# Kernel optimization log

Hardware: AMD Instinct MI355X
Metric: run time of the kernel (lower is better)

## Reference

```python
import jax, jax.numpy as jnp
import numpy as np

EPS = 1e-5
BATCH = 2
VOX_H = 8  # grid resolution at depth - stages = 3


def conv_bn_relu(x, neigh, W, gamma, beta):
    # octree sparse conv: gather 27 neighbors per node, then GEMM
    N = neigh.shape[0]
    g = x[neigh].reshape(N, -1)              # [N, 27*Cin]
    y = g @ W                                # [N, Cout]
    mean = jnp.mean(y, axis=0)
    var = jnp.var(y, axis=0)
    y = (y - mean) * jax.lax.rsqrt(var + EPS) * gamma + beta
    return jax.nn.relu(y)


def octree_max_pool(x):
    # max over 8 sibling children -> parent node
    return x.reshape(-1, 8, x.shape[-1]).max(axis=1)


def setup_inputs() -> dict:
    key = jax.random.key(0)
    ks = jax.random.split(key, 8)
    N6, N5, N4, N3 = 524288, 65536, 8192, 1024
    inp = {
        "data": jax.random.normal(ks[0], (N6, 4), jnp.float32),
        "W0": jax.random.normal(ks[1], (108, 16), jnp.float32) * 0.1,
        "g0": jnp.ones((16,), jnp.float32),
        "b0": jnp.zeros((16,), jnp.float32),
        "W1": jax.random.normal(ks[2], (432, 32), jnp.float32) * 0.05,
        "g1": jnp.ones((32,), jnp.float32),
        "b1": jnp.zeros((32,), jnp.float32),
        "W2": jax.random.normal(ks[3], (864, 64), jnp.float32) * 0.05,
        "g2": jnp.ones((64,), jnp.float32),
        "b2": jnp.zeros((64,), jnp.float32),
        "neigh0": jax.random.randint(ks[4], (N6, 27), 0, N6, jnp.int32),
        "neigh1": jax.random.randint(ks[5], (N5, 27), 0, N5, jnp.int32),
        "neigh2": jax.random.randint(ks[6], (N4, 27), 0, N4, jnp.int32),
        "vox_idx": jnp.arange(N3, dtype=jnp.int32),
        "depth": 6,
    }
    return inp


def reference(data, W0, g0, b0, W1, g1, b1, W2, g2, b2,
              neigh0, neigh1, neigh2, vox_idx, depth):
    x = conv_bn_relu(data, neigh0, W0, g0, b0)
    x = octree_max_pool(x)
    x = conv_bn_relu(x, neigh1, W1, g1, b1)
    x = octree_max_pool(x)
    x = conv_bn_relu(x, neigh2, W2, g2, b2)
    x = octree_max_pool(x)                   # [N3, 64]
    # octree2voxel: scatter node features into dense grid per batch sample
    C = x.shape[-1]
    vox = jnp.zeros((BATCH * VOX_H ** 3, C), x.dtype).at[vox_idx].set(x)
    vox = vox.reshape(BATCH, VOX_H, VOX_H, VOX_H, C)
    return vox.transpose(0, 4, 1, 2, 3)      # [B, C, H, H, H]
```

## Files before the change

kernel.cpp:

```cpp
#include <hip/hip_runtime.h>

#define BN_EPS 1e-5f
#define NBUF 64

typedef float        f32x4 __attribute__((ext_vector_type(4)));
typedef float        f32x2 __attribute__((ext_vector_type(2)));
typedef unsigned int u32x2 __attribute__((ext_vector_type(2)));
typedef unsigned int u32x4 __attribute__((ext_vector_type(4)));

__device__ inline unsigned pack_bf16(float a, float b) {
    unsigned ua = __float_as_uint(a);
    unsigned ub = __float_as_uint(b);
    ua = (ua + 0x7fffu + ((ua >> 16) & 1u)) >> 16;
    ub = (ub + 0x7fffu + ((ub >> 16) & 1u)) >> 16;
    return ua | (ub << 16);
}
__device__ inline float bf_lo(unsigned u) { return __uint_as_float(u << 16); }
__device__ inline float bf_hi(unsigned u) { return __uint_as_float(u & 0xffff0000u); }

__global__ void __launch_bounds__(256) cast_bf16_kernel(
    const f32x4* __restrict__ in, u32x2* __restrict__ out, int n4)
{
    const int t = blockIdx.x * 256 + threadIdx.x;
    if (t >= n4) return;
    const f32x4 v = in[t];
    u32x2 r;
    r.x = pack_bf16(v.x, v.y);
    r.y = pack_bf16(v.z, v.w);
    out[t] = r;
}

__global__ void __launch_bounds__(256) conv0_kernel(
    const unsigned long long* __restrict__ xb, const int* __restrict__ neigh,
    const float* __restrict__ W, float* __restrict__ y,
    float* __restrict__ stats)
{
    __shared__ float Wlds[27 * 4 * 16];
    for (int i = threadIdx.x; i < 27 * 4 * 16; i += 256) Wlds[i] = W[i];
    __syncthreads();

    const int node = blockIdx.x * 256 + threadIdx.x;
    const int* nrow = neigh + (size_t)node * 27;

    int idx[27];
#pragma unroll
    for (int j = 0; j < 27; ++j) idx[j] = __builtin_nontemporal_load(nrow + j);

    float acc[16];
#pragma unroll
    for (int c = 0; c < 16; ++c) acc[c] = 0.f;

#pragma unroll
    for (int g = 0; g < 27; g += 9) {
        unsigned long long xr[9];
#pragma unroll
        for (int u = 0; u < 9; ++u)
            xr[u] = __hip_atomic_load(xb + idx[g + u], __ATOMIC_RELAXED,
                                      __HIP_MEMORY_SCOPE_AGENT);
#pragma unroll
        for (int u = 0; u < 9; ++u) {
            const int j = g + u;
            const unsigned lo = (unsigned)xr[u];
            const unsigned hi = (unsigned)(xr[u] >> 32);
            float xv[4];
            xv[0] = bf_lo(lo); xv[1] = bf_hi(lo);
            xv[2] = bf_lo(hi); xv[3] = bf_hi(hi);
#pragma unroll
            for (int kk = 0; kk < 4; ++kk) {
                const f32x4* wv = (const f32x4*)&Wlds[(j * 4 + kk) * 16];
#pragma unroll
                for (int c4 = 0; c4 < 4; ++c4) {
                    const f32x4 w = wv[c4];
                    acc[c4 * 4 + 0] = fmaf(xv[kk], w.x, acc[c4 * 4 + 0]);
                    acc[c4 * 4 + 1] = fmaf(xv[kk], w.y, acc[c4 * 4 + 1]);
                    acc[c4 * 4 + 2] = fmaf(xv[kk], w.z, acc[c4 * 4 + 2]);
                    acc[c4 * 4 + 3] = fmaf(xv[kk], w.w, acc[c4 * 4 + 3]);
                }
            }
        }
    }

    f32x4* yr = (f32x4*)(y + (size_t)node * 16);
#pragma unroll
    for (int c4 = 0; c4 < 4; ++c4) {
        f32x4 v = { acc[c4 * 4 + 0], acc[c4 * 4 + 1], acc[c4 * 4 + 2], acc[c4 * 4 + 3] };
        __builtin_nontemporal_store(v, yr + c4);
    }

    float* buf = stats + (blockIdx.x & (NBUF - 1)) * (2 * 16);
#pragma unroll
    for (int c = 0; c < 16; ++c) {
        float v = acc[c];
        float q = v * v;
#pragma unroll
        for (int off = 32; off > 0; off >>= 1) {
            v += __shfl_xor(v, off, 64);
            q += __shfl_xor(q, off, 64);
        }
        if ((threadIdx.x & 63) == 0) {
            atomicAdd(&buf[c], v);
            atomicAdd(&buf[16 + c], q);
        }
    }
}

__global__ void __launch_bounds__(256) conv1_kernel(
    const u32x4* __restrict__ xb, const int* __restrict__ neigh,
    const float* __restrict__ W, float* __restrict__ y,
    float* __restrict__ stats)
{
    __shared__ float Wlds[27 * 16 * 8];
    const int cobase = blockIdx.y * 8;

    for (int i = threadIdx.x; i < 27 * 16 * 8; i += 256) {
        int k = i >> 3, c = i & 7;
        Wlds[i] = W[k * 32 + cobase + c];
    }
    __syncthreads();

    const int node = blockIdx.x * 256 + threadIdx.x;
    const int* nrow = neigh + (size_t)node * 27;

    int idx[27];
#pragma unroll
    for (int j = 0; j < 27; ++j) idx[j] = __builtin_nontemporal_load(nrow + j);

    float acc[8];
#pragma unroll
    for (int c = 0; c < 8; ++c) acc[c] = 0.f;

#pragma unroll 1
    for (int g = 0; g < 27; g += 3) {
        u32x4 xa[3], xc[3];
#pragma unroll
        for (int u = 0; u < 3; ++u) {
            const size_t r = (size_t)idx[g + u] * 2;
            xa[u] = xb[r];
            xc[u] = xb[r + 1];
        }
#pragma unroll
        for (int u = 0; u < 3; ++u) {
            const int j = g + u;
            float xv[16];
            xv[0]  = bf_lo(xa[u].x); xv[1]  = bf_hi(xa[u].x);
            xv[2]  = bf_lo(xa[u].y); xv[3]  = bf_hi(xa[u].y);
            xv[4]  = bf_lo(xa[u].z); xv[5]  = bf_hi(xa[u].z);
            xv[6]  = bf_lo(xa[u].w); xv[7]  = bf_hi(xa[u].w);
            xv[8]  = bf_lo(xc[u].x); xv[9]  = bf_hi(xc[u].x);
            xv[10] = bf_lo(xc[u].y); xv[11] = bf_hi(xc[u].y);
            xv[12] = bf_lo(xc[u].z); xv[13] = bf_hi(xc[u].z);
            xv[14] = bf_lo(xc[u].w); xv[15] = bf_hi(xc[u].w);
#pragma unroll
            for (int k = 0; k < 16; ++k) {
                const f32x4* wv = (const f32x4*)&Wlds[(j * 16 + k) * 8];
#pragma unroll
                for (int c4 = 0; c4 < 2; ++c4) {
                    const f32x4 w = wv[c4];
                    acc[c4 * 4 + 0] = fmaf(xv[k], w.x, acc[c4 * 4 + 0]);
                    acc[c4 * 4 + 1] = fmaf(xv[k], w.y, acc[c4 * 4 + 1]);
                    acc[c4 * 4 + 2] = fmaf(xv[k], w.z, acc[c4 * 4 + 2]);
                    acc[c4 * 4 + 3] = fmaf(xv[k], w.w, acc[c4 * 4 + 3]);
                }
            }
        }
    }

    f32x4* yr = (f32x4*)(y + (size_t)node * 32 + cobase);
#pragma unroll
    for (int c4 = 0; c4 < 2; ++c4) {
        f32x4 v = { acc[c4 * 4 + 0], acc[c4 * 4 + 1], acc[c4 * 4 + 2], acc[c4 * 4 + 3] };
        __builtin_nontemporal_store(v, yr + c4);
    }

    float* buf = stats + (blockIdx.x & (NBUF - 1)) * (2 * 32);
#pragma unroll
    for (int c = 0; c < 8; ++c) {
        float v = acc[c];
        float q = v * v;
#pragma unroll
        for (int off = 32; off > 0; off >>= 1) {
            v += __shfl_xor(v, off, 64);
            q += __shfl_xor(q, off, 64);
        }
        if ((threadIdx.x & 63) == 0) {
            atomicAdd(&buf[cobase + c], v);
            atomicAdd(&buf[32 + cobase + c], q);
        }
    }
}

__global__ void __launch_bounds__(256) conv2_kernel(
    const u32x4* __restrict__ xb, const int* __restrict__ neigh,
    const float* __restrict__ W, float* __restrict__ y,
    float* __restrict__ stats)
{
    __shared__ int idxlds[16 * 27];
    const int nbase = blockIdx.x * 16;
    for (int i = threadIdx.x; i < 16 * 27; i += 256) {
        int n = i / 27, j = i - n * 27;
        idxlds[i] = __builtin_nontemporal_load(neigh + (size_t)(nbase + n) * 27 + j);
    }
    __syncthreads();

    const int ln = threadIdx.x >> 4;
    const int c4 = threadIdx.x & 15;
    const int node = nbase + ln;

    f32x4 acc = { 0.f, 0.f, 0.f, 0.f };

#pragma unroll 1
    for (int j = 0; j < 27; ++j) {
        const int nb = idxlds[ln * 27 + j];
        const u32x4* xr = xb + (size_t)nb * 4;
        u32x4 xq[4];
#pragma unroll
        for (int q = 0; q < 4; ++q) xq[q] = xr[q];
#pragma unroll
        for (int q = 0; q < 4; ++q) {
            float xv[8];
            xv[0] = bf_lo(xq[q].x); xv[1] = bf_hi(xq[q].x);
            xv[2] = bf_lo(xq[q].y); xv[3] = bf_hi(xq[q].y);
            xv[4] = bf_lo(xq[q].z); xv[5] = bf_hi(xq[q].z);
            xv[6] = bf_lo(xq[q].w); xv[7] = bf_hi(xq[q].w);
#pragma unroll
            for (int h = 0; h < 8; ++h) {
                const int k = q * 8 + h;
                const f32x4 w = *(const f32x4*)(W + ((size_t)j * 32 + k) * 64 + c4 * 4);
                acc.x = fmaf(xv[h], w.x, acc.x);
                acc.y = fmaf(xv[h], w.y, acc.y);
                acc.z = fmaf(xv[h], w.z, acc.z);
                acc.w = fmaf(xv[h], w.w, acc.w);
            }
        }
    }

    __builtin_nontemporal_store(acc, (f32x4*)(y + (size_t)node * 64 + c4 * 4));

    float sx = acc.x, sy = acc.y, sz = acc.z, sw = acc.w;
    float qx = acc.x * acc.x, qy = acc.y * acc.y, qz = acc.z * acc.z, qw = acc.w * acc.w;
#pragma unroll
    for (int off = 16; off <= 32; off <<= 1) {
        sx += __shfl_xor(sx, off, 64);  sy += __shfl_xor(sy, off, 64);
        sz += __shfl_xor(sz, off, 64);  sw += __shfl_xor(sw, off, 64);
        qx += __shfl_xor(qx, off, 64);  qy += __shfl_xor(qy, off, 64);
        qz += __shfl_xor(qz, off, 64);  qw += __shfl_xor(qw, off, 64);
    }
    if ((threadIdx.x & 63) < 16) {
        float* buf = stats + (blockIdx.x & (NBUF - 1)) * (2 * 64);
        atomicAdd(&buf[c4 * 4 + 0], sx);
        atomicAdd(&buf[c4 * 4 + 1], sy);
        atomicAdd(&buf[c4 * 4 + 2], sz);
        atomicAdd(&buf[c4 * 4 + 3], sw);
        atomicAdd(&buf[64 + c4 * 4 + 0], qx);
        atomicAdd(&buf[64 + c4 * 4 + 1], qy);
        atomicAdd(&buf[64 + c4 * 4 + 2], qz);
        atomicAdd(&buf[64 + c4 * 4 + 3], qw);
    }
}

template<int COUT, bool BF16OUT>
__global__ void __launch_bounds__(256) pool_fin_kernel(
    const float* __restrict__ y, const float* __restrict__ stats,
    const float* __restrict__ gamma, const float* __restrict__ beta,
    void* __restrict__ xout, float invN, int total2)
{
    __shared__ float ss[2 * COUT];
    if (threadIdx.x < COUT) {
        const int c = threadIdx.x;
        float s = 0.f, q = 0.f;
        for (int b = 0; b < NBUF; ++b) {
            s += stats[b * 2 * COUT + c];
            q += stats[b * 2 * COUT + COUT + c];
        }
        const float mean = s * invN;
        const float var  = fmaf(-mean, mean, q * invN);
        const float sc   = gamma[c] * rsqrtf(var + BN_EPS);
        ss[c]        = sc;
        ss[COUT + c] = fmaf(-mean, sc, beta[c]);
    }
    __syncthreads();

    const int t = blockIdx.x * 256 + threadIdx.x;
    if (t >= total2) return;
    const int p  = t / (COUT / 2);
    const int c2 = (t % (COUT / 2)) * 2;
    const float sc0 = ss[c2],     sh0 = ss[COUT + c2];
    const float sc1 = ss[c2 + 1], sh1 = ss[COUT + c2 + 1];
    const float* yr = y + (size_t)p * 8 * COUT + c2;
    float m0 = -3.4e38f, m1 = -3.4e38f;
#pragma unroll
    for (int i = 0; i < 8; ++i) {
        const f32x2 v = __builtin_nontemporal_load((const f32x2*)(yr + i * COUT));
        m0 = fmaxf(m0, fmaf(v.x, sc0, sh0));
        m1 = fmaxf(m1, fmaf(v.y, sc1, sh1));
    }
    m0 = fmaxf(m0, 0.f);
    m1 = fmaxf(m1, 0.f);
    if (BF16OUT) {
        ((unsigned*)xout)[t] = pack_bf16(m0, m1);
    } else {
        f32x2 r = { m0, m1 };
        ((f32x2*)xout)[t] = r;
    }
}

__global__ void __launch_bounds__(256) scatter_kernel(
    const float* __restrict__ x3, const int* __restrict__ vox,
    float* __restrict__ out)
{
    const int t = blockIdx.x * 256 + threadIdx.x;
    const int n = t >> 6, c = t & 63;
    const int r = vox[n];
    out[((r >> 9) << 15) + (c << 9) + (r & 511)] = x3[t];
}

extern "C" void kernel_launch(void* const* d_in, const int* in_sizes, int n_in,
                              void* d_out, int out_size, void* d_ws, size_t ws_size,
                              hipStream_t stream)
{
    const float* data = (const float*)d_in[0];
    const float* W0   = (const float*)d_in[1];
    const float* g0   = (const float*)d_in[2];
    const float* b0   = (const float*)d_in[3];
    const float* W1   = (const float*)d_in[4];
    const float* g1   = (const float*)d_in[5];
    const float* b1   = (const float*)d_in[6];
    const float* W2   = (const float*)d_in[7];
    const float* g2   = (const float*)d_in[8];
    const float* b2   = (const float*)d_in[9];
    const int* neigh0 = (const int*)d_in[10];
    const int* neigh1 = (const int*)d_in[11];
    const int* neigh2 = (const int*)d_in[12];
    const int* vox    = (const int*)d_in[13];

    const int N6 = 524288, N5 = 65536, N4 = 8192, N3 = 1024;

    float* ws = (float*)d_ws;
    const size_t off_y0  = 0;
    const size_t off_xb1 = off_y0 + (size_t)N6 * 16;
    const size_t off_y1  = off_xb1 + (size_t)N5 * 8;
    const size_t off_xb0 = off_y1;
    const size_t off_xb2 = off_y1 + (size_t)N5 * 32;
    const size_t off_y2  = off_xb2 + (size_t)N4 * 16;
    const size_t off_x3  = off_y2 + (size_t)N4 * 64;
    const size_t off_st0 = off_x3 + (size_t)N3 * 64;
    const size_t off_st1 = off_st0 + NBUF * 2 * 16;
    const size_t off_st2 = off_st1 + NBUF * 2 * 32;

    (void)hipMemsetAsync(ws + off_st0, 0, (size_t)(NBUF * 2 * (16 + 32 + 64)) * sizeof(float), stream);

    cast_bf16_kernel<<<N6 / 256, 256, 0, stream>>>(
        (const f32x4*)data, (u32x2*)(ws + off_xb0), N6);
    conv0_kernel<<<N6 / 256, 256, 0, stream>>>(
        (const unsigned long long*)(ws + off_xb0), neigh0, W0, ws + off_y0, ws + off_st0);
    pool_fin_kernel<16, true><<<(N5 * 8) / 256, 256, 0, stream>>>(
        ws + off_y0, ws + off_st0, g0, b0, ws + off_xb1, 1.f / N6, N5 * 8);

    conv1_kernel<<<dim3(N5 / 256, 4), 256, 0, stream>>>(
        (const u32x4*)(ws + off_xb1), neigh1, W1, ws + off_y1, ws + off_st1);
    pool_fin_kernel<32, true><<<(N4 * 16) / 256, 256, 0, stream>>>(
        ws + off_y1, ws + off_st1, g1, b1, ws + off_xb2, 1.f / N5, N4 * 16);

    conv2_kernel<<<N4 / 16, 256, 0, stream>>>(
        (const u32x4*)(ws + off_xb2), neigh2, W2, ws + off_y2, ws + off_st2);
    pool_fin_kernel<64, false><<<(N3 * 32) / 256, 256, 0, stream>>>(
        ws + off_y2, ws + off_st2, g2, b2, ws + off_x3, 1.f / N4, N3 * 32);

    (void)hipMemsetAsync(d_out, 0, (size_t)out_size * sizeof(float), stream);
    scatter_kernel<<<(N3 * 64) / 256, 256, 0, stream>>>(ws + off_x3, vox, (float*)d_out);
}
```

Baseline: 275.9 us.

## Stage neighbor indices in LDS and restructure conv1 to split neighbors across half-blocks

conv0 now loads each block's neighbor index rows into LDS with coalesced reads, issues all 27 gathers up front, and reads weights from global memory (uniform, likely served from scalar cache) instead of staging them in LDS. conv1 drops the 4-way output-channel grid split, so each node's neighbors are gathered once instead of four times. In its place, two threads per node each handle about half the 27 neighbors across all 32 output channels, and the partial sums are combined through LDS. This removes redundant gathers but raises register pressure (28 u32x4 plus 32 accumulators) and adds an LDS reduction with two extra barriers.

```diff
diff --git a/kernel.cpp b/kernel.cpp
--- a/kernel.cpp
+++ b/kernel.cpp
@@ -35,47 +35,45 @@
     const float* __restrict__ W, float* __restrict__ y,
     float* __restrict__ stats)
 {
-    __shared__ float Wlds[27 * 4 * 16];
-    for (int i = threadIdx.x; i < 27 * 4 * 16; i += 256) Wlds[i] = W[i];
+    __shared__ int idxlds[256 * 27];
+    {
+        const size_t base = (size_t)blockIdx.x * (256 * 27);
+        for (int i = threadIdx.x; i < 256 * 27; i += 256)
+            idxlds[i] = neigh[base + i];
+    }
     __syncthreads();
 
     const int node = blockIdx.x * 256 + threadIdx.x;
-    const int* nrow = neigh + (size_t)node * 27;
-
-    int idx[27];
-#pragma unroll
-    for (int j = 0; j < 27; ++j) idx[j] = __builtin_nontemporal_load(nrow + j);
+
+    unsigned long long xr[27];
+#pragma unroll
+    for (int j = 0; j < 27; ++j) {
+        const int nb = idxlds[threadIdx.x * 27 + j];
+        xr[j] = __hip_atomic_load(xb + nb, __ATOMIC_RELAXED,
+                                  __HIP_MEMORY_SCOPE_AGENT);
+    }
 
     float acc[16];
 #pragma unroll
     for (int c = 0; c < 16; ++c) acc[c] = 0.f;
 
 #pragma unroll
-    for (int g = 0; g < 27; g += 9) {
-        unsigned long long xr[9];
-#pragma unroll
-        for (int u = 0; u < 9; ++u)
-            xr[u] = __hip_atomic_load(xb + idx[g + u], __ATOMIC_RELAXED,
-                                      __HIP_MEMORY_SCOPE_AGENT);
-#pragma unroll
-        for (int u = 0; u < 9; ++u) {
-            const int j = g + u;
-            const unsigned lo = (unsigned)xr[u];
-            const unsigned hi = (unsigned)(xr[u] >> 32);
-            float xv[4];
-            xv[0] = bf_lo(lo); xv[1] = bf_hi(lo);
-            xv[2] = bf_lo(hi); xv[3] = bf_hi(hi);
-#pragma unroll
-            for (int kk = 0; kk < 4; ++kk) {
-                const f32x4* wv = (const f32x4*)&Wlds[(j * 4 + kk) * 16];
-#pragma unroll
-                for (int c4 = 0; c4 < 4; ++c4) {
-                    const f32x4 w = wv[c4];
-                    acc[c4 * 4 + 0] = fmaf(xv[kk], w.x, acc[c4 * 4 + 0]);
-                    acc[c4 * 4 + 1] = fmaf(xv[kk], w.y, acc[c4 * 4 + 1]);
-                    acc[c4 * 4 + 2] = fmaf(xv[kk], w.z, acc[c4 * 4 + 2]);
-                    acc[c4 * 4 + 3] = fmaf(xv[kk], w.w, acc[c4 * 4 + 3]);
-                }
+    for (int j = 0; j < 27; ++j) {
+        const unsigned lo = (unsigned)xr[j];
+        const unsigned hi = (unsigned)(xr[j] >> 32);
+        float xv[4];
+        xv[0] = bf_lo(lo); xv[1] = bf_hi(lo);
+        xv[2] = bf_lo(hi); xv[3] = bf_hi(hi);
+#pragma unroll
+        for (int kk = 0; kk < 4; ++kk) {
+            const f32x4* wr = (const f32x4*)(W + (j * 4 + kk) * 16);
+#pragma unroll
+            for (int c4 = 0; c4 < 4; ++c4) {
+                const f32x4 w = wr[c4];
+                acc[c4 * 4 + 0] = fmaf(xv[kk], w.x, acc[c4 * 4 + 0]);
+                acc[c4 * 4 + 1] = fmaf(xv[kk], w.y, acc[c4 * 4 + 1]);
+                acc[c4 * 4 + 2] = fmaf(xv[kk], w.z, acc[c4 * 4 + 2]);
+                acc[c4 * 4 + 3] = fmaf(xv[kk], w.w, acc[c4 * 4 + 3]);
             }
         }
     }
@@ -109,53 +107,53 @@
     const float* __restrict__ W, float* __restrict__ y,
     float* __restrict__ stats)
 {
-    __shared__ float Wlds[27 * 16 * 8];
-    const int cobase = blockIdx.y * 8;
-
-    for (int i = threadIdx.x; i < 27 * 16 * 8; i += 256) {
-        int k = i >> 3, c = i & 7;
-        Wlds[i] = W[k * 32 + cobase + c];
-    }
-    __syncthreads();
-
-    const int node = blockIdx.x * 256 + threadIdx.x;
-    const int* nrow = neigh + (size_t)node * 27;
-
-    int idx[27];
-#pragma unroll
-    for (int j = 0; j < 27; ++j) idx[j] = __builtin_nontemporal_load(nrow + j);
-
-    float acc[8];
-#pragma unroll
-    for (int c = 0; c < 8; ++c) acc[c] = 0.f;
-
-#pragma unroll 1
-    for (int g = 0; g < 27; g += 3) {
-        u32x4 xa[3], xc[3];
-#pragma unroll
-        for (int u = 0; u < 3; ++u) {
-            const size_t r = (size_t)idx[g + u] * 2;
-            xa[u] = xb[r];
-            xc[u] = xb[r + 1];
-        }
-#pragma unroll
-        for (int u = 0; u < 3; ++u) {
-            const int j = g + u;
+    __shared__ int sh[128 * 33];
+    int*   idxlds = sh;
+    float* red    = (float*)sh;
+
+    const int nbase = blockIdx.x * 128;
+    for (int i = threadIdx.x; i < 128 * 27; i += 256)
+        idxlds[i] = neigh[(size_t)nbase * 27 + i];
+    __syncthreads();
+
+    const int ln   = threadIdx.x & 127;
+    const int half = threadIdx.x >> 7;
+    const int node = nbase + ln;
+    const int js   = half ? 14 : 0;
+    const int nj   = half ? 13 : 14;
+
+    u32x4 xa[14], xc[14];
+#pragma unroll
+    for (int jj = 0; jj < 14; ++jj) {
+        const int j = js + ((jj < nj) ? jj : 0);
+        const size_t r = (size_t)idxlds[ln * 27 + j] * 2;
+        xa[jj] = xb[r];
+        xc[jj] = xb[r + 1];
+    }
+
+    float acc[32];
+#pragma unroll
+    for (int c = 0; c < 32; ++c) acc[c] = 0.f;
+
+#pragma unroll
+    for (int jj = 0; jj < 14; ++jj) {
+        if (jj < nj) {
+            const int j = js + jj;
             float xv[16];
-            xv[0]  = bf_lo(xa[u].x); xv[1]  = bf_hi(xa[u].x);
-            xv[2]  = bf_lo(xa[u].y); xv[3]  = bf_hi(xa[u].y);
-            xv[4]  = bf_lo(xa[u].z); xv[5]  = bf_hi(xa[u].z);
-            xv[6]  = bf_lo(xa[u].w); xv[7]  = bf_hi(xa[u].w);
-            xv[8]  = bf_lo(xc[u].x); xv[9]  = bf_hi(xc[u].x);
-            xv[10] = bf_lo(xc[u].y); xv[11] = bf_hi(xc[u].y);
-            xv[12] = bf_lo(xc[u].z); xv[13] = bf_hi(xc[u].z);
-            xv[14] = bf_lo(xc[u].w); xv[15] = bf_hi(xc[u].w);
+            xv[0]  = bf_lo(xa[jj].x); xv[1]  = bf_hi(xa[jj].x);
+            xv[2]  = bf_lo(xa[jj].y); xv[3]  = bf_hi(xa[jj].y);
+            xv[4]  = bf_lo(xa[jj].z); xv[5]  = bf_hi(xa[jj].z);
+            xv[6]  = bf_lo(xa[jj].w); xv[7]  = bf_hi(xa[jj].w);
+            xv[8]  = bf_lo(xc[jj].x); xv[9]  = bf_hi(xc[jj].x);
+            xv[10] = bf_lo(xc[jj].y); xv[11] = bf_hi(xc[jj].y);
+            xv[12] = bf_lo(xc[jj].z); xv[13] = bf_hi(xc[jj].z);
+            xv[14] = bf_lo(xc[jj].w); xv[15] = bf_hi(xc[jj].w);
 #pragma unroll
             for (int k = 0; k < 16; ++k) {
-                const f32x4* wv = (const f32x4*)&Wlds[(j * 16 + k) * 8];
-#pragma unroll
-                for (int c4 = 0; c4 < 2; ++c4) {
-                    const f32x4 w = wv[c4];
+                const f32x4* wr = (const f32x4*)(W + ((size_t)(j * 16 + k)) * 32);
+#pragma unroll
+                for (int c4 = 0; c4 < 8; ++c4) {
+                    const f32x4 w = wr[c4];
                     acc[c4 * 4 + 0] = fmaf(xv[k], w.x, acc[c4 * 4 + 0]);
                     acc[c4 * 4 + 1] = fmaf(xv[k], w.y, acc[c4 * 4 + 1]);
                     acc[c4 * 4 + 2] = fmaf(xv[k], w.z, acc[c4 * 4 + 2]);
@@ -165,26 +163,37 @@
         }
     }
 
-    f32x4* yr = (f32x4*)(y + (size_t)node * 32 + cobase);
-#pragma unroll
-    for (int c4 = 0; c4 < 2; ++c4) {
-        f32x4 v = { acc[c4 * 4 + 0], acc[c4 * 4 + 1], acc[c4 * 4 + 2], acc[c4 * 4 + 3] };
-        __builtin_nontemporal_store(v, yr + c4);
-    }
-
-    float* buf = stats + (blockIdx.x & (NBUF - 1)) * (2 * 32);
-#pragma unroll
-    for (int c = 0; c < 8; ++c) {
-        float v = acc[c];
-        float q = v * v;
-#pragma unroll
-        for (int off = 32; off > 0; off >>= 1) {
-            v += __shfl_xor(v, off, 64);
-            q += __shfl_xor(q, off, 64);
-        }
-        if ((threadIdx.x & 63) == 0) {
-            atomicAdd(&buf[cobase + c], v);
-            atomicAdd(&buf[32 + cobase + c], q);
+    __syncthreads();
+    if (half) {
+#pragma unroll
+        for (int c = 0; c < 32; ++c) red[ln * 33 + c] = acc[c];
+    }
+    __syncthreads();
+    if (!half) {
+#pragma unroll
+        for (int c = 0; c < 32; ++c) acc[c] += red[ln * 33 + c];
+
+        f32x4* yr = (f32x4*)(y + (size_t)node * 32);
+#pragma unroll
+        for (int c4 = 0; c4 < 8; ++c4) {
+            f32x4 v = { acc[c4 * 4 + 0], acc[c4 * 4 + 1], acc[c4 * 4 + 2], acc[c4 * 4 + 3] };
+            __builtin_nontemporal_store(v, yr + c4);
+        }
+
+        float* buf = stats + (blockIdx.x & (NBUF - 1)) * (2 * 32);
+#pragma unroll
+        for (int c = 0; c < 32; ++c) {
+            float v = acc[c];
+            float q = v * v;
+#pragma unroll
+            for (int off = 32; off > 0; off >>= 1) {
+                v += __shfl_xor(v, off, 64);
+                q += __shfl_xor(q, off, 64);
+            }
+            if ((threadIdx.x & 63) == 0) {
+                atomicAdd(&buf[c], v);
+                atomicAdd(&buf[32 + c], q);
+            }
         }
     }
 }
@@ -198,7 +207,7 @@
     const int nbase = blockIdx.x * 16;
     for (int i = threadIdx.x; i < 16 * 27; i += 256) {
         int n = i / 27, j = i - n * 27;
-        idxlds[i] = __builtin_nontemporal_load(neigh + (size_t)(nbase + n) * 27 + j);
+        idxlds[i] = neigh[(size_t)(nbase + n) * 27 + j];
     }
     __syncthreads();
 
@@ -356,7 +365,7 @@
     pool_fin_kernel<16, true><<<(N5 * 8) / 256, 256, 0, stream>>>(
         ws + off_y0, ws + off_st0, g0, b0, ws + off_xb1, 1.f / N6, N5 * 8);
 
-    conv1_kernel<<<dim3(N5 / 256, 4), 256, 0, stream>>>(
+    conv1_kernel<<<N5 / 128, 256, 0, stream>>>(
         (const u32x4*)(ws + off_xb1), neigh1, W1, ws + off_y1, ws + off_st1);
     pool_fin_kernel<32, true><<<(N4 * 16) / 256, 256, 0, stream>>>(
         ws + off_y1, ws + off_st1, g1, b1, ws + off_xb2, 1.f / N5, N4 * 16);
```

Result: slower. 313.9 us (+13.8%).
